# Kernel optimization log

Measured on AMD Instinct MI355X. Metric: run time of the kernel, lower is better.

The kernel has to match this reference:

```python
import jax, jax.numpy as jnp
import numpy as np

BS, P, D, D_WM, H, W = 64, 512, 1024, 1024, 16, 128
HD = D_WM // H
SCALE = 1.0 / np.sqrt(HD)


def setup_inputs() -> dict:
    key = jax.random.key(0)
    ks = jax.random.split(key, 10)
    s = 0.02
    x_all = jax.random.normal(ks[0], (BS, P, D), dtype=jnp.float32)
    reset_mask_all = jax.random.randint(ks[1], (BS, P), 0, 50) == 0
    return {
        'x_all': x_all,
        'reset_mask_all': reset_mask_all,
        'Wq_w': jax.random.normal(ks[2], (D, D_WM), dtype=jnp.float32) * s,
        'Wq_b': jnp.zeros((D_WM,), jnp.float32),
        'Wk_w': jax.random.normal(ks[3], (D, D_WM), dtype=jnp.float32) * s,
        'Wk_b': jnp.zeros((D_WM,), jnp.float32),
        'Wv_w': jax.random.normal(ks[4], (D, D_WM), dtype=jnp.float32) * s,
        'Wv_b': jnp.zeros((D_WM,), jnp.float32),
        'Wo_w': jax.random.normal(ks[5], (D_WM, D), dtype=jnp.float32) * s,
        'Wo_b': jnp.zeros((D,), jnp.float32),
    }


def _forward_span(x_all, reset_mask_all, Wq_w, Wq_b, Wk_w, Wk_b, Wv_w, Wv_b, Wo_w, Wo_b):
    # Batched projections over all P tokens (matches forward_span)
    q_all = jnp.einsum('bpd,de->bpe', x_all, Wq_w) + Wq_b
    k_all = jnp.einsum('bpd,de->bpe', x_all, Wk_w) + Wk_b
    v_all = jnp.einsum('bpd,de->bpe', x_all, Wv_w) + Wv_b

    def step(carry, inp):
        K, V, valid, ptr = carry  # [BS,W,D_WM], [BS,W,D_WM], [BS,W] bool, [BS] int
        q, k, v, reset_t = inp    # [BS,D_WM] x3, [BS] bool
        # doc-boundary reset
        valid = valid & ~reset_t[:, None]
        ptr = jnp.where(reset_t, 0, ptr)
        # ring-buffer write at ptr (one-hot broadcast, as in the original)
        wm = jnp.arange(W)[None, :] == ptr[:, None]          # [BS,W] bool
        wf = wm.astype(K.dtype)[:, :, None]                   # [BS,W,1]
        K = K * (1.0 - wf) + k[:, None, :] * wf
        V = V * (1.0 - wf) + v[:, None, :] * wf
        valid = valid | wm
        # windowed multi-head attention over the buffer
        qh = q.reshape(BS, H, HD)
        Kh = K.reshape(BS, W, H, HD)
        Vh = V.reshape(BS, W, H, HD)
        attn = jnp.einsum('bhd,bwhd->bhw', qh, Kh) * SCALE
        attn = jnp.where(valid[:, None, :], attn, -jnp.inf)
        attn = jax.nn.softmax(attn, axis=-1)
        attn = jnp.nan_to_num(attn)
        out = jnp.einsum('bhw,bwhd->bhd', attn, Vh).reshape(BS, D_WM)
        y = out @ Wo_w + Wo_b
        ptr = (ptr + 1) % W
        return (K, V, valid, ptr), y

    init = (
        jnp.zeros((BS, W, D_WM), x_all.dtype),
        jnp.zeros((BS, W, D_WM), x_all.dtype),
        jnp.zeros((BS, W), bool),
        jnp.zeros((BS,), jnp.int32),
    )
    xs = (
        q_all.transpose(1, 0, 2),
        k_all.transpose(1, 0, 2),
        v_all.transpose(1, 0, 2),
        reset_mask_all.T,
    )
    _, ys = jax.lax.scan(step, init, xs)  # ys: [P,BS,D]
    return ys.transpose(1, 0, 2)


def reference(x_all, reset_mask_all, Wq_w, Wq_b, Wk_w, Wk_b, Wv_w, Wv_b, Wo_w, Wo_b):
    return _forward_span(x_all, reset_mask_all, Wq_w, Wq_b, Wk_w, Wk_b, Wv_w, Wv_b, Wo_w, Wo_b)
```

## Files before the change

kernel.cpp:

```cpp
#include <hip/hip_runtime.h>
#include <stdint.h>

typedef __bf16 bf16_t;
typedef __bf16 bf16x8 __attribute__((ext_vector_type(8)));
typedef __bf16 bf16x4 __attribute__((ext_vector_type(4)));
typedef float  f32x4  __attribute__((ext_vector_type(4)));

constexpr int cBS = 64, cP = 512, cD = 1024, cDWM = 1024, cH = 16, cHD = 64, cW = 128;
constexpr int cVTP = 672;
constexpr int cM = cBS * cP;
constexpr float cSCALE = 0.125f;

__device__ __forceinline__ void gld_lds16(const void* g, void* l) {
#if __has_builtin(__builtin_amdgcn_global_load_lds)
  __builtin_amdgcn_global_load_lds(
      (__attribute__((address_space(1))) void*)g,
      (__attribute__((address_space(3))) void*)l, 16, 0, 0);
#else
  *(bf16x8*)l = *(const bf16x8*)g;
#endif
}

__global__ void cvt_x_k(const float* __restrict__ X, bf16_t* __restrict__ Y, int n) {
  int i = (blockIdx.x * blockDim.x + threadIdx.x) * 4;
  if (i >= n) return;
  float4 v = *(const float4*)(X + i);
  bf16x4 o;
  o[0] = (bf16_t)v.x; o[1] = (bf16_t)v.y; o[2] = (bf16_t)v.z; o[3] = (bf16_t)v.w;
  *(bf16x4*)(Y + i) = o;
}

__global__ void cvt_wt_k(const float* __restrict__ W0, const float* __restrict__ W1,
                         const float* __restrict__ W2, const float* __restrict__ W3,
                         bf16_t* __restrict__ T0, bf16_t* __restrict__ T1,
                         bf16_t* __restrict__ T2, bf16_t* __restrict__ T3) {
  __shared__ float tile[32][33];
  const float* Wsrc; bf16_t* Tdst;
  switch (blockIdx.z) {
    case 0: Wsrc = W0; Tdst = T0; break;
    case 1: Wsrc = W1; Tdst = T1; break;
    case 2: Wsrc = W2; Tdst = T2; break;
    default: Wsrc = W3; Tdst = T3; break;
  }
  const int n0 = blockIdx.x * 32, k0 = blockIdx.y * 32;
  const int c = threadIdx.x & 31, r8 = threadIdx.x >> 5;
#pragma unroll
  for (int q = 0; q < 4; ++q) {
    int row = r8 + q * 8;
    tile[row][c] = Wsrc[(size_t)(k0 + row) * 1024 + n0 + c];
  }
  __syncthreads();
#pragma unroll
  for (int q = 0; q < 4; ++q) {
    int row = r8 + q * 8;
    Tdst[(size_t)(n0 + row) * 1024 + k0 + c] = (bf16_t)tile[c][row];
  }
}

__global__ void resets2_k(const int* __restrict__ mask, int* __restrict__ r) {
  __shared__ int sm[cP];
  const int b = blockIdx.x, t = threadIdx.x;
  sm[t] = mask[b * cP + t] ? t : 0;
  __syncthreads();
#pragma unroll
  for (int d = 1; d < cP; d <<= 1) {
    int u = (t >= d) ? sm[t - d] : 0;
    __syncthreads();
    if (u > sm[t]) sm[t] = u;
    __syncthreads();
  }
  r[b * cP + t] = sm[t];
}

__global__ __launch_bounds__(512, 2)
void gemm_qkv8_k(const bf16_t* __restrict__ A, const bf16_t* __restrict__ Wt,
                 const float* __restrict__ bq, const float* __restrict__ bk,
                 const float* __restrict__ bvv,
                 bf16_t* __restrict__ Qh, bf16_t* __restrict__ Kh,
                 bf16_t* __restrict__ Vt) {
  __shared__ __align__(16) char LDS[131072];
  const int tid = threadIdx.x;
  const int wid = tid >> 6, ln = tid & 63;
  const int ln15 = ln & 15, g4 = ln >> 4;
  const int wr = wid >> 2, wc = wid & 3;

  const int g = blockIdx.x + 12 * blockIdx.y;
  const int xcd = g & 7, s = g >> 3;
  const int nb = s % 12, mloc = s / 12;
  const int m0 = (xcd * 16 + mloc) * 256, n0 = nb * 256;

  const bf16_t* Ab = A + (size_t)m0 * 1024;
  const bf16_t* Bb = Wt + (size_t)n0 * 1024;

  const int srow = (tid >> 6) * 16 + (tid & 15);
  const int kc = (tid >> 4) & 3;
  const size_t aoff = (size_t)srow * 1024 + (size_t)(kc * 8);
  char* const lbase = LDS + tid * 16;

  const int lane16 = (g4 * 16 + ln15) * 16;
  const int abase = (wr * 8) * 1024 + lane16;
  const int bbase = (wc * 4) * 1024 + lane16;

  f32x4 acc[8][4];
#pragma unroll
  for (int i = 0; i < 8; ++i)
#pragma unroll
    for (int j = 0; j < 4; ++j) acc[i][j] = {0.f, 0.f, 0.f, 0.f};

#define STAGE_A(buf, kh, j) do {                                              \
    const bf16_t* gp_ = Ab + (size_t)((j) * 64 + (kh) * 32) + aoff;           \
    char* lp_ = lbase + (buf) * 65536 + (kh) * 16384;                         \
    gld_lds16(gp_, lp_);                                                      \
    gld_lds16(gp_ + (size_t)128 * 1024, lp_ + 8192);                          \
  } while (0)

#define STAGE_B(buf, kh, j) do {                                              \
    const bf16_t* gp_ = Bb + (size_t)((j) * 64 + (kh) * 32) + aoff;           \
    char* lp_ = lbase + (buf) * 65536 + (kh) * 16384 + 32768;                 \
    gld_lds16(gp_, lp_);                                                      \
    gld_lds16(gp_ + (size_t)128 * 1024, lp_ + 8192);                          \
  } while (0)

#define NOSTAGE ((void)0)
#define VM4 asm volatile("s_waitcnt vmcnt(4)" ::: "memory")
#define VM0 asm volatile("s_waitcnt vmcnt(0)" ::: "memory")
#define NOVM ((void)0)

#define PHASE(buf, kh, STAGE, VME) do {                                       \
    const char* Ar_ = LDS + (buf) * 65536 + (kh) * 16384 + abase;             \
    const char* Br_ = LDS + (buf) * 65536 + (kh) * 16384 + 32768 + bbase;     \
    bf16x8 af_[8], bf_[4];                                                    \
    _Pragma("unroll")                                                         \
    for (int nj_ = 0; nj_ < 4; ++nj_)                                         \
      bf_[nj_] = *(const bf16x8*)(Br_ + nj_ * 1024);                          \
    _Pragma("unroll")                                                         \
    for (int mi_ = 0; mi_ < 8; ++mi_)                                         \
      af_[mi_] = *(const bf16x8*)(Ar_ + mi_ * 1024);                          \
    STAGE;                                                                    \
    __builtin_amdgcn_s_setprio(1);                                            \
    _Pragma("unroll")                                                         \
    for (int mi_ = 0; mi_ < 8; ++mi_)                                         \
      _Pragma("unroll")                                                       \
      for (int nj_ = 0; nj_ < 4; ++nj_)                                       \
        acc[mi_][nj_] = __builtin_amdgcn_mfma_f32_16x16x32_bf16(              \
            af_[mi_], bf_[nj_], acc[mi_][nj_], 0, 0, 0);                      \
    __builtin_amdgcn_s_setprio(0);                                            \
    VME;                                                                      \
    __builtin_amdgcn_s_barrier();                                             \
    __builtin_amdgcn_sched_barrier(0);                                        \
  } while (0)

  STAGE_A(0, 0, 0); STAGE_B(0, 0, 0);
  STAGE_A(0, 1, 0); STAGE_B(0, 1, 0);
  VM4;
  __builtin_amdgcn_s_barrier();
  __builtin_amdgcn_sched_barrier(0);

  for (int t = 0; t < 7; ++t) {
    const int j1 = 2 * t + 1, j2 = 2 * t + 2;
    PHASE(0, 0, { STAGE_A(1, 0, j1); STAGE_B(1, 0, j1); }, VM4);
    PHASE(0, 1, { STAGE_A(1, 1, j1); STAGE_B(1, 1, j1); }, VM4);
    PHASE(1, 0, { STAGE_A(0, 0, j2); STAGE_B(0, 0, j2); }, VM4);
    PHASE(1, 1, { STAGE_A(0, 1, j2); STAGE_B(0, 1, j2); }, VM4);
  }
  PHASE(0, 0, { STAGE_A(1, 0, 15); STAGE_B(1, 0, 15); }, VM4);
  PHASE(0, 1, { STAGE_A(1, 1, 15); STAGE_B(1, 1, 15); }, VM4);
  PHASE(1, 0, NOSTAGE, VM0);
  PHASE(1, 1, NOSTAGE, NOVM);

#undef PHASE
#undef STAGE_A
#undef STAGE_B

  const int seg = n0 >> 10;
  const float* bias = (seg == 0) ? bq : (seg == 1) ? bk : bvv;
  bf16_t* QK = (seg == 0) ? Qh : Kh;
#pragma unroll
  for (int mi = 0; mi < 8; ++mi) {
    const int rbase = m0 + wr * 128 + mi * 16 + g4 * 4;
    const int b = rbase >> 9, pb = rbase & 511;
#pragma unroll
    for (int nj = 0; nj < 4; ++nj) {
      const int col = n0 + wc * 64 + nj * 16 + ln15;
      const int cl = col & 1023;
      const int h = cl >> 6, hd = cl & 63;
      const float bv = bias[cl];
      if (seg < 2) {
#pragma unroll
        for (int r = 0; r < 4; ++r)
          QK[(((size_t)(b * cH + h)) * cP + pb + r) * cHD + hd] =
              (bf16_t)(acc[mi][nj][r] + bv);
      } else {
        bf16x4 pk;
#pragma unroll
        for (int r = 0; r < 4; ++r) pk[r] = (bf16_t)(acc[mi][nj][r] + bv);
        *(bf16x4*)(Vt + ((size_t)((b * cH + h) * cHD + hd)) * cVTP + 128 + pb) = pk;
      }
    }
  }
}

__global__ __launch_bounds__(256)
void gemm_bt_k(const bf16_t* __restrict__ A, const bf16_t* __restrict__ Bt,
               const float* __restrict__ bias, float* __restrict__ C,
               int M, int N, int K) {
  __shared__ __align__(16) bf16_t As[2][128 * 32];
  __shared__ __align__(16) bf16_t Bs[2][128 * 32];
  const int tid = threadIdx.x;
  const int wv = tid >> 6, ln = tid & 63;
  const int ln15 = ln & 15, g4 = ln >> 4;

  const int g = blockIdx.x + 8 * blockIdx.y;
  const int xcd = g & 7, s = g >> 3;
  const int nb = s & 7, mloc = s >> 3;
  const int m0 = (xcd * 32 + mloc) * 128, n0 = nb * 128;

  const int wm = (wv >> 1) * 64, wn = (wv & 1) * 64;
  const bf16_t* Ab = A + (size_t)m0 * K;
  const bf16_t* Bb = Bt + (size_t)n0 * K;

  auto stage = [&](const bf16_t* G, bf16_t* L, int k0) {
#pragma unroll
    for (int gg = 0; gg < 2; ++gg) {
      int slot = gg * 256 + tid;
      gld_lds16(G + (size_t)(slot >> 2) * K + (k0 + (slot & 3) * 8), L + slot * 8);
    }
  };

  f32x4 acc[4][4];
#pragma unroll
  for (int i = 0; i < 4; ++i)
#pragma unroll
    for (int j = 0; j < 4; ++j) acc[i][j] = {0.f, 0.f, 0.f, 0.f};

  const int nk = K >> 5;
  stage(Ab, As[0], 0);
  stage(Bb, Bs[0], 0);
  for (int kt = 0; kt < nk; ++kt) {
    __syncthreads();
    if (kt + 1 < nk) {
      stage(Ab, As[(kt + 1) & 1], (kt + 1) * 32);
      stage(Bb, Bs[(kt + 1) & 1], (kt + 1) * 32);
    }
    const bf16_t* Asb = As[kt & 1];
    const bf16_t* Bsb = Bs[kt & 1];
    bf16x8 af[4], bfr[4];
#pragma unroll
    for (int i = 0; i < 4; ++i)
      af[i] = *(const bf16x8*)(Asb + (wm + i * 16 + ln15) * 32 + g4 * 8);
#pragma unroll
    for (int j = 0; j < 4; ++j)
      bfr[j] = *(const bf16x8*)(Bsb + (wn + j * 16 + ln15) * 32 + g4 * 8);
#pragma unroll
    for (int i = 0; i < 4; ++i)
#pragma unroll
      for (int j = 0; j < 4; ++j)
        acc[i][j] = __builtin_amdgcn_mfma_f32_16x16x32_bf16(af[i], bfr[j], acc[i][j], 0, 0, 0);
  }

#pragma unroll
  for (int i = 0; i < 4; ++i) {
    const int rbase = m0 + wm + i * 16 + g4 * 4;
#pragma unroll
    for (int j = 0; j < 4; ++j) {
      const int col = n0 + wn + j * 16 + ln15;
      const float bv = bias[col];
#pragma unroll
      for (int r = 0; r < 4; ++r)
        C[(size_t)(rbase + r) * N + col] = acc[i][j][r] + bv;
    }
  }
}

__global__ __launch_bounds__(256)
void attn3_k(const bf16_t* __restrict__ Q, const bf16_t* __restrict__ Kv,
             const bf16_t* __restrict__ Vt, const int* __restrict__ rr,
             bf16_t* __restrict__ O) {
  __shared__ __align__(16) bf16_t Pl[4][16][168];
  const int tid = threadIdx.x;
  const int wv = tid >> 6, ln = tid & 63, ln15 = ln & 15, g4 = ln >> 4;
  const int h = blockIdx.x, b = blockIdx.y, tc = blockIdx.z;
  bf16_t(*Pw)[168] = Pl[wv];
  const bf16_t* vb = Vt + ((size_t)(b * cH + h)) * cHD * cVTP;
  const bf16_t* qb = Q + ((size_t)(b * cH + h)) * cP * cHD;
  const bf16_t* kb = Kv + ((size_t)(b * cH + h)) * cP * cHD;

  for (int sub = 0; sub < 2; ++sub) {
    const int t0 = (tc * 2 + sub) * 64 + wv * 16;
    const int sbase = t0 - 128;

    int rv[4];
#pragma unroll
    for (int r = 0; r < 4; ++r) rv[r] = rr[b * cP + t0 + g4 * 4 + r];

    const bf16_t* qp = qb + (size_t)(t0 + ln15) * cHD + g4 * 8;
    const bf16x8 qa0 = *(const bf16x8*)qp;
    const bf16x8 qa1 = *(const bf16x8*)(qp + 32);

    f32x4 lg[9];
#pragma unroll
    for (int c = 0; c < 9; ++c) {
      const int s = sbase + c * 16 + ln15;
      bf16x8 k0v, k1v;
      if ((unsigned)s < (unsigned)cP) {
        const bf16_t* kp = kb + (size_t)s * cHD + g4 * 8;
        k0v = *(const bf16x8*)kp;
        k1v = *(const bf16x8*)(kp + 32);
      } else {
#pragma unroll
        for (int z = 0; z < 8; ++z) { k0v[z] = (bf16_t)0.f; k1v[z] = (bf16_t)0.f; }
      }
      f32x4 a = {0.f, 0.f, 0.f, 0.f};
      a = __builtin_amdgcn_mfma_f32_16x16x32_bf16(qa0, k0v, a, 0, 0, 0);
      a = __builtin_amdgcn_mfma_f32_16x16x32_bf16(qa1, k1v, a, 0, 0, 0);
      lg[c] = a;
    }

    float mx[4] = {-1e30f, -1e30f, -1e30f, -1e30f};
#pragma unroll
    for (int c = 0; c < 9; ++c)
#pragma unroll
      for (int r = 0; r < 4; ++r) {
        const int s = sbase + c * 16 + ln15;
        const int t = t0 + g4 * 4 + r;
        const bool ok = (s >= rv[r]) && (s <= t) && (t - s < cW);
        const float l = ok ? lg[c][r] * cSCALE : -1e30f;
        lg[c][r] = l;
        mx[r] = fmaxf(mx[r], l);
      }
#pragma unroll
    for (int r = 0; r < 4; ++r) {
      mx[r] = fmaxf(mx[r], __shfl_xor(mx[r], 1));
      mx[r] = fmaxf(mx[r], __shfl_xor(mx[r], 2));
      mx[r] = fmaxf(mx[r], __shfl_xor(mx[r], 4));
      mx[r] = fmaxf(mx[r], __shfl_xor(mx[r], 8));
    }
    float sm[4] = {0.f, 0.f, 0.f, 0.f};
#pragma unroll
    for (int c = 0; c < 9; ++c)
#pragma unroll
      for (int r = 0; r < 4; ++r) {
        const float e = __expf(lg[c][r] - mx[r]);
        lg[c][r] = e;
        sm[r] += e;
      }
#pragma unroll
    for (int r = 0; r < 4; ++r) {
      sm[r] += __shfl_xor(sm[r], 1);
      sm[r] += __shfl_xor(sm[r], 2);
      sm[r] += __shfl_xor(sm[r], 4);
      sm[r] += __shfl_xor(sm[r], 8);
    }
    float inv[4];
#pragma unroll
    for (int r = 0; r < 4; ++r) inv[r] = 1.f / sm[r];

#pragma unroll
    for (int c = 0; c < 9; ++c)
#pragma unroll
      for (int r = 0; r < 4; ++r)
        Pw[g4 * 4 + r][c * 16 + ln15] = (bf16_t)(lg[c][r] * inv[r]);
#pragma unroll
    for (int z = 0; z < 4; ++z)
      Pw[ln15][144 + g4 * 4 + z] = (bf16_t)0.f;

    f32x4 oacc[4];
#pragma unroll
    for (int j = 0; j < 4; ++j) oacc[j] = {0.f, 0.f, 0.f, 0.f};
#pragma unroll
    for (int c2 = 0; c2 < 5; ++c2) {
      const bf16x8 pa = *(const bf16x8*)(&Pw[ln15][c2 * 32 + g4 * 8]);
#pragma unroll
      for (int j = 0; j < 4; ++j) {
        const bf16x8 vf =
            *(const bf16x8*)(vb + (size_t)(j * 16 + ln15) * cVTP + (t0 + c2 * 32 + g4 * 8));
        oacc[j] = __builtin_amdgcn_mfma_f32_16x16x32_bf16(pa, vf, oacc[j], 0, 0, 0);
      }
    }
#pragma unroll
    for (int j = 0; j < 4; ++j) {
      const int col = h * cHD + j * 16 + ln15;
#pragma unroll
      for (int r = 0; r < 4; ++r)
        O[((size_t)(b * cP + t0 + g4 * 4 + r)) * cDWM + col] = (bf16_t)oacc[j][r];
    }
  }
}

extern "C" void kernel_launch(void* const* d_in, const int* in_sizes, int n_in,
                              void* d_out, int out_size, void* d_ws, size_t ws_size,
                              hipStream_t stream) {
  (void)in_sizes; (void)n_in; (void)out_size; (void)ws_size;
  const float* x  = (const float*)d_in[0];
  const int* mask = (const int*)d_in[1];
  const float* Wq = (const float*)d_in[2];
  const float* bq = (const float*)d_in[3];
  const float* Wk = (const float*)d_in[4];
  const float* bk = (const float*)d_in[5];
  const float* Wv = (const float*)d_in[6];
  const float* bv = (const float*)d_in[7];
  const float* Wo = (const float*)d_in[8];
  const float* bo = (const float*)d_in[9];
  float* out = (float*)d_out;

  char* ws = (char*)d_ws;
  size_t off = 0;
  bf16_t* Xbf = (bf16_t*)(ws + off); off += (size_t)cM * cD * 2;
  bf16_t* Wqt = (bf16_t*)(ws + off); off += (size_t)cD * cDWM * 2;
  bf16_t* Wkt = (bf16_t*)(ws + off); off += (size_t)cD * cDWM * 2;
  bf16_t* Wvt = (bf16_t*)(ws + off); off += (size_t)cD * cDWM * 2;
  bf16_t* Wot = (bf16_t*)(ws + off); off += (size_t)cDWM * cD * 2;
  bf16_t* Qh  = (bf16_t*)(ws + off); off += (size_t)cM * cDWM * 2;
  bf16_t* Kh  = (bf16_t*)(ws + off); off += (size_t)cM * cDWM * 2;
  bf16_t* Vt  = (bf16_t*)(ws + off); off += (size_t)cBS * cH * cHD * cVTP * 2;
  int* rbuf   = (int*)(ws + off);    off += (size_t)cBS * cP * 4;
  bf16_t* Ob  = Xbf;

  cvt_x_k<<<(cM * cD / 4 + 255) / 256, 256, 0, stream>>>(x, Xbf, cM * cD);
  cvt_wt_k<<<dim3(32, 32, 4), 256, 0, stream>>>(Wq, Wk, Wv, Wo, Wqt, Wkt, Wvt, Wot);
  resets2_k<<<cBS, cP, 0, stream>>>(mask, rbuf);

  gemm_qkv8_k<<<dim3(12, 128), 512, 0, stream>>>(Xbf, Wqt, bq, bk, bv, Qh, Kh, Vt);

  attn3_k<<<dim3(cH, cBS, 4), 256, 0, stream>>>(Qh, Kh, Vt, rbuf, Ob);

  gemm_bt_k<<<dim3(8, 256), 256, 0, stream>>>(Ob, Wot, bo, out, cM, cD, cDWM);
}
```

Measured before the change: 540.0 us.

## Shrink QKV GEMM tile to 256x128 with triple-buffered K=32 pipeline

The fused QKV projection GEMM moves from 256x256 tiles with double-buffered K=64 stages to 256x128 tiles with triple-buffered K=32 stages. LDS drops from 128KB to 72KB and per-wave accumulators halve, with launch bounds raised to allow more resident blocks per CU. The grid doubles along N. The aim is more occupancy and deeper prefetch to hide memory latency, at the cost of lower arithmetic intensity per tile and more A-tile reloads from global memory.

```diff
diff --git a/kernel.cpp b/kernel.cpp
--- a/kernel.cpp
+++ b/kernel.cpp
@@ -72,22 +72,22 @@
   r[b * cP + t] = sm[t];
 }
 
-__global__ __launch_bounds__(512, 2)
+__global__ __launch_bounds__(512, 4)
 void gemm_qkv8_k(const bf16_t* __restrict__ A, const bf16_t* __restrict__ Wt,
                  const float* __restrict__ bq, const float* __restrict__ bk,
                  const float* __restrict__ bvv,
                  bf16_t* __restrict__ Qh, bf16_t* __restrict__ Kh,
                  bf16_t* __restrict__ Vt) {
-  __shared__ __align__(16) char LDS[131072];
+  __shared__ __align__(16) char LDS[73728];
   const int tid = threadIdx.x;
   const int wid = tid >> 6, ln = tid & 63;
   const int ln15 = ln & 15, g4 = ln >> 4;
-  const int wr = wid >> 2, wc = wid & 3;
-
-  const int g = blockIdx.x + 12 * blockIdx.y;
+  const int wr = wid >> 1, wc = wid & 1;
+
+  const int g = blockIdx.x + 24 * blockIdx.y;
   const int xcd = g & 7, s = g >> 3;
-  const int nb = s % 12, mloc = s / 12;
-  const int m0 = (xcd * 16 + mloc) * 256, n0 = nb * 256;
+  const int nb = s % 24, mloc = s / 24;
+  const int m0 = (xcd * 16 + mloc) * 256, n0 = nb * 128;
 
   const bf16_t* Ab = A + (size_t)m0 * 1024;
   const bf16_t* Bb = Wt + (size_t)n0 * 1024;
@@ -98,48 +98,43 @@
   char* const lbase = LDS + tid * 16;
 
   const int lane16 = (g4 * 16 + ln15) * 16;
-  const int abase = (wr * 8) * 1024 + lane16;
-  const int bbase = (wc * 4) * 1024 + lane16;
-
-  f32x4 acc[8][4];
-#pragma unroll
-  for (int i = 0; i < 8; ++i)
+  const int abase = (wr * 4) * 1024 + lane16;
+  const int bbase = 16384 + (wc * 4) * 1024 + lane16;
+
+  f32x4 acc[4][4];
+#pragma unroll
+  for (int i = 0; i < 4; ++i)
 #pragma unroll
     for (int j = 0; j < 4; ++j) acc[i][j] = {0.f, 0.f, 0.f, 0.f};
 
-#define STAGE_A(buf, kh, j) do {                                              \
-    const bf16_t* gp_ = Ab + (size_t)((j) * 64 + (kh) * 32) + aoff;           \
-    char* lp_ = lbase + (buf) * 65536 + (kh) * 16384;                         \
-    gld_lds16(gp_, lp_);                                                      \
-    gld_lds16(gp_ + (size_t)128 * 1024, lp_ + 8192);                          \
+#define STAGE(buf, j) do {                                                    \
+    const bf16_t* gA_ = Ab + (size_t)((j) * 32) + aoff;                       \
+    const bf16_t* gB_ = Bb + (size_t)((j) * 32) + aoff;                       \
+    char* lp_ = lbase + (buf) * 24576;                                        \
+    gld_lds16(gA_, lp_);                                                      \
+    gld_lds16(gA_ + (size_t)128 * 1024, lp_ + 8192);                          \
+    gld_lds16(gB_, lp_ + 16384);                                              \
   } while (0)
 
-#define STAGE_B(buf, kh, j) do {                                              \
-    const bf16_t* gp_ = Bb + (size_t)((j) * 64 + (kh) * 32) + aoff;           \
-    char* lp_ = lbase + (buf) * 65536 + (kh) * 16384 + 32768;                 \
-    gld_lds16(gp_, lp_);                                                      \
-    gld_lds16(gp_ + (size_t)128 * 1024, lp_ + 8192);                          \
-  } while (0)
-
 #define NOSTAGE ((void)0)
-#define VM4 asm volatile("s_waitcnt vmcnt(4)" ::: "memory")
+#define VM3 asm volatile("s_waitcnt vmcnt(3)" ::: "memory")
 #define VM0 asm volatile("s_waitcnt vmcnt(0)" ::: "memory")
 #define NOVM ((void)0)
 
-#define PHASE(buf, kh, STAGE, VME) do {                                       \
-    const char* Ar_ = LDS + (buf) * 65536 + (kh) * 16384 + abase;             \
-    const char* Br_ = LDS + (buf) * 65536 + (kh) * 16384 + 32768 + bbase;     \
-    bf16x8 af_[8], bf_[4];                                                    \
+#define PHASE(buf, STAGE_, VME) do {                                          \
+    const char* Ar_ = LDS + (buf) * 24576 + abase;                            \
+    const char* Br_ = LDS + (buf) * 24576 + bbase;                            \
+    bf16x8 af_[4], bf_[4];                                                    \
     _Pragma("unroll")                                                         \
     for (int nj_ = 0; nj_ < 4; ++nj_)                                         \
       bf_[nj_] = *(const bf16x8*)(Br_ + nj_ * 1024);                          \
     _Pragma("unroll")                                                         \
-    for (int mi_ = 0; mi_ < 8; ++mi_)                                         \
+    for (int mi_ = 0; mi_ < 4; ++mi_)                                         \
       af_[mi_] = *(const bf16x8*)(Ar_ + mi_ * 1024);                          \
-    STAGE;                                                                    \
+    STAGE_;                                                                   \
     __builtin_amdgcn_s_setprio(1);                                            \
     _Pragma("unroll")                                                         \
-    for (int mi_ = 0; mi_ < 8; ++mi_)                                         \
+    for (int mi_ = 0; mi_ < 4; ++mi_)                                         \
       _Pragma("unroll")                                                       \
       for (int nj_ = 0; nj_ < 4; ++nj_)                                       \
         acc[mi_][nj_] = __builtin_amdgcn_mfma_f32_16x16x32_bf16(              \
@@ -150,34 +145,30 @@
     __builtin_amdgcn_sched_barrier(0);                                        \
   } while (0)
 
-  STAGE_A(0, 0, 0); STAGE_B(0, 0, 0);
-  STAGE_A(0, 1, 0); STAGE_B(0, 1, 0);
-  VM4;
+  STAGE(0, 0);
+  STAGE(1, 1);
+  VM3;
   __builtin_amdgcn_s_barrier();
   __builtin_amdgcn_sched_barrier(0);
 
-  for (int t = 0; t < 7; ++t) {
-    const int j1 = 2 * t + 1, j2 = 2 * t + 2;
-    PHASE(0, 0, { STAGE_A(1, 0, j1); STAGE_B(1, 0, j1); }, VM4);
-    PHASE(0, 1, { STAGE_A(1, 1, j1); STAGE_B(1, 1, j1); }, VM4);
-    PHASE(1, 0, { STAGE_A(0, 0, j2); STAGE_B(0, 0, j2); }, VM4);
-    PHASE(1, 1, { STAGE_A(0, 1, j2); STAGE_B(0, 1, j2); }, VM4);
-  }
-  PHASE(0, 0, { STAGE_A(1, 0, 15); STAGE_B(1, 0, 15); }, VM4);
-  PHASE(0, 1, { STAGE_A(1, 1, 15); STAGE_B(1, 1, 15); }, VM4);
-  PHASE(1, 0, NOSTAGE, VM0);
-  PHASE(1, 1, NOSTAGE, NOVM);
+  for (int t = 0; t < 10; ++t) {
+    const int j = 3 * t;
+    PHASE(0, STAGE(2, j + 2), VM3);
+    PHASE(1, STAGE(0, j + 3), VM3);
+    PHASE(2, STAGE(1, j + 4), VM3);
+  }
+  PHASE(0, NOSTAGE, VM0);
+  PHASE(1, NOSTAGE, NOVM);
 
 #undef PHASE
-#undef STAGE_A
-#undef STAGE_B
+#undef STAGE
 
   const int seg = n0 >> 10;
   const float* bias = (seg == 0) ? bq : (seg == 1) ? bk : bvv;
   bf16_t* QK = (seg == 0) ? Qh : Kh;
 #pragma unroll
-  for (int mi = 0; mi < 8; ++mi) {
-    const int rbase = m0 + wr * 128 + mi * 16 + g4 * 4;
+  for (int mi = 0; mi < 4; ++mi) {
+    const int rbase = m0 + wr * 64 + mi * 16 + g4 * 4;
     const int b = rbase >> 9, pb = rbase & 511;
 #pragma unroll
     for (int nj = 0; nj < 4; ++nj) {
@@ -420,7 +411,7 @@
   cvt_wt_k<<<dim3(32, 32, 4), 256, 0, stream>>>(Wq, Wk, Wv, Wo, Wqt, Wkt, Wvt, Wot);
   resets2_k<<<cBS, cP, 0, stream>>>(mask, rbuf);
 
-  gemm_qkv8_k<<<dim3(12, 128), 512, 0, stream>>>(Xbf, Wqt, bq, bk, bv, Qh, Kh, Vt);
+  gemm_qkv8_k<<<dim3(24, 128), 512, 0, stream>>>(Xbf, Wqt, bq, bk, bv, Qh, Kh, Vt);
 
   attn3_k<<<dim3(cH, cBS, 4), 256, 0, stream>>>(Qh, Kh, Vt, rbuf, Ob);
 
```

New measurement: 594.5 us. 1.1x slower.
